# Kernel tuning notes

Measured on AMD Instinct MI355X. Metric: run time of the kernel, lower is better.

## Reference

```python
import jax, jax.numpy as jnp
import numpy as np

D_MODEL = 1024
EXPAND = 2
D_INNER = D_MODEL * EXPAND  # 2048
D_STATE = 16
D_CONV = 4
DT_RANK = max(16, D_MODEL // 16)  # 64
BATCH = 1
SEQ = 2048


def _hippo_eigvals(N):
    # HiPPO-LegS matrix: A[n,m] = -(2*max(n,m)+1)
    n = np.arange(N)
    A = -(2.0 * np.maximum(n[:, None], n[None, :]) + 1.0)
    w, _ = np.linalg.eigh(A)
    idx = np.argsort(np.abs(w))[::-1]
    return w[idx]


def setup_inputs() -> dict:
    key = jax.random.key(0)
    ks = jax.random.split(key, 10)
    s = 0.02
    return {
        "x": jax.random.normal(ks[0], (BATCH, SEQ, D_MODEL), jnp.float32),
        "in_w": jax.random.normal(ks[1], (D_MODEL, D_INNER), jnp.float32) * s,
        "in_b": jnp.zeros((D_INNER,), jnp.float32),
        "conv_w": jax.random.normal(ks[2], (D_INNER, 1, D_CONV), jnp.float32) * s,
        "conv_b": jnp.zeros((D_INNER,), jnp.float32),
        "A_log": jnp.asarray(np.log(np.abs(_hippo_eigvals(D_STATE))), jnp.float32),
        "B_mat": jax.random.normal(ks[3], (D_STATE, D_INNER), jnp.float32) * s,
        "C_mat": jax.random.normal(ks[4], (D_STATE, D_INNER), jnp.float32) * s,
        "D_vec": jnp.ones((D_INNER,), jnp.float32),
        "gate_w": jax.random.normal(ks[5], (D_MODEL, D_INNER), jnp.float32) * s,
        "gate_b": jnp.zeros((D_INNER,), jnp.float32),
        "dt1_w": jax.random.normal(ks[6], (D_INNER, DT_RANK), jnp.float32) * s,
        "dt1_b": jnp.zeros((DT_RANK,), jnp.float32),
        "dt2_w": jax.random.normal(ks[7], (DT_RANK, D_INNER), jnp.float32) * s,
        "dt2_b": jnp.full((D_INNER,), -4.0, jnp.float32),  # softplus -> small dt
        "out_w": jax.random.normal(ks[8], (D_INNER, D_MODEL), jnp.float32) * s,
        "out_b": jnp.zeros((D_MODEL,), jnp.float32),
    }


def reference(x, in_w, in_b, conv_w, conv_b, A_log, B_mat, C_mat, D_vec,
              gate_w, gate_b, dt1_w, dt1_b, dt2_w, dt2_b, out_w, out_b):
    B, L, _ = x.shape
    u = x @ in_w + in_b  # (B, L, D_INNER)
    # causal depthwise conv1d: left-pad d_conv-1 (torch pads both sides then trims to L)
    uc = jax.lax.conv_general_dilated(
        u.transpose(0, 2, 1), conv_w, (1,), [(D_CONV - 1, 0)],
        dimension_numbers=("NCH", "OIH", "NCH"),
        feature_group_count=D_INNER) + conv_b[None, :, None]
    u = jax.nn.silu(uc.transpose(0, 2, 1))  # (B, L, D_INNER)
    # input-dependent time step via low-rank dt projection
    delta = jax.nn.softplus((u @ dt1_w + dt1_b) @ dt2_w + dt2_b)  # (B, L, D_INNER)
    # ZOH discretization of diagonal A (matches discretize_zoh diagonal branch)
    A = -jnp.exp(A_log)  # (N,)
    dA = delta[..., None] * A  # (B, L, D, N)
    A_bar = jnp.exp(dA)
    safe_A = jnp.where(jnp.abs(A) < 1e-6, 1.0, A)
    expansion = jnp.where(jnp.abs(A) < 1e-6,
                          delta[..., None] * (1.0 + 0.5 * dA),
                          (A_bar - 1.0) / safe_A)  # (B, L, D, N)
    Bu = expansion * B_mat.T[None, None, :, :] * u[..., None]  # (B, L, D, N)
    # sequential state recurrence h[k] = A_bar[k] * h[k-1] + B_bar[k] * u[k]
    def step(h, ab_bu):
        ab, bu = ab_bu
        h = ab * h + bu
        return h, h
    h0 = jnp.zeros((B, D_INNER, D_STATE), x.dtype)
    _, hs = jax.lax.scan(step, h0, (A_bar.transpose(1, 0, 2, 3), Bu.transpose(1, 0, 2, 3)))
    hs = hs.transpose(1, 0, 2, 3)  # (B, L, D, N)
    y = jnp.einsum("bldn,nd->bld", hs, C_mat) + D_vec * u
    y = y * jax.nn.silu(x @ gate_w + gate_b)
    return y @ out_w + out_b
```

## Files before the change

kernel.cpp:

```cpp
#include <hip/hip_runtime.h>

#define L_SEQ 2048
#define DM    1024
#define DI    2048
#define NS    16
#define DTR   64
#define CH    128
#define CL    16
#define KZ_DT 16
#define KZ_OUT 4

typedef short bf16x8_t __attribute__((ext_vector_type(8)));
typedef float f32x4    __attribute__((ext_vector_type(4)));

__device__ __forceinline__ unsigned short f2bf(float f) {
    union { float f; unsigned int u; } v; v.f = f;
    unsigned int u = v.u;
    unsigned int r = (u + 0x7FFFu + ((u >> 16) & 1u)) >> 16;
    return (unsigned short)r;
}

__global__ void cast_bf16_kernel(const float* __restrict__ in,
                                 unsigned short* __restrict__ out, int n) {
    int i = (blockIdx.x * blockDim.x + threadIdx.x) * 4;
    if (i + 3 < n) {
        float4 v = *(const float4*)&in[i];
        ushort4 o;
        o.x = f2bf(v.x); o.y = f2bf(v.y); o.z = f2bf(v.z); o.w = f2bf(v.w);
        *(ushort4*)&out[i] = o;
    }
}

__global__ void tcast_kernel(const float* __restrict__ in,
                             unsigned short* __restrict__ out, int K, int N) {
    __shared__ float tile[32][33];
    int tx = threadIdx.x & 31, ty = threadIdx.x >> 5;
    int n0 = blockIdx.x * 32, k0 = blockIdx.y * 32;
    #pragma unroll
    for (int i = ty; i < 32; i += 8) {
        int k = k0 + i, n = n0 + tx;
        tile[i][tx] = (k < K && n < N) ? in[(size_t)k * N + n] : 0.f;
    }
    __syncthreads();
    #pragma unroll
    for (int i = ty; i < 32; i += 8) {
        int n = n0 + i, k = k0 + tx;
        if (n < N && k < K) out[(size_t)n * K + k] = f2bf(tile[tx][i]);
    }
}

__global__ __launch_bounds__(256, 2)
void gemm_bf16(const unsigned short* __restrict__ A,
               const unsigned short* __restrict__ Bt,
               float* __restrict__ C,
               const float* __restrict__ bias0, const float* __restrict__ bias1,
               int bsplit, int M, int Ntot, int K, int kchunk) {
    __shared__ short As[128][40];
    __shared__ short Bs[128][40];
    const int tid  = threadIdx.x;
    const int bm   = blockIdx.y * 128, bn = blockIdx.x * 128;
    const int lane = tid & 63, wave = tid >> 6;
    const int wm   = (wave >> 1) * 64, wn = (wave & 1) * 64;
    const int quad = lane >> 4, r16 = lane & 15;

    f32x4 acc[4][4];
    #pragma unroll
    for (int i = 0; i < 4; i++)
        #pragma unroll
        for (int j = 0; j < 4; j++)
            #pragma unroll
            for (int r = 0; r < 4; r++) acc[i][j][r] = 0.f;

    const int lrow = tid >> 2;
    const int lcol = (tid & 3) * 8;
    const short* agp = (const short*)A + (size_t)(bm + lrow) * K + lcol;
    const short* bgp = (const short*)Bt + (size_t)(bn + lrow) * K + lcol;
    const size_t rstep = (size_t)64 * K;

    const int kbase  = blockIdx.z * kchunk;
    const int kiters = kchunk / 32;

    int kcur = kbase;
    bf16x8_t na0 = *(const bf16x8_t*)(agp + kcur);
    bf16x8_t na1 = *(const bf16x8_t*)(agp + rstep + kcur);
    bf16x8_t nb0 = *(const bf16x8_t*)(bgp + kcur);
    bf16x8_t nb1 = *(const bf16x8_t*)(bgp + rstep + kcur);

    for (int it = 0; it < kiters; ++it) {
        *(bf16x8_t*)&As[lrow][lcol]      = na0;
        *(bf16x8_t*)&As[lrow + 64][lcol] = na1;
        *(bf16x8_t*)&Bs[lrow][lcol]      = nb0;
        *(bf16x8_t*)&Bs[lrow + 64][lcol] = nb1;
        __syncthreads();

        int kn = (it + 1 < kiters) ? kcur + 32 : kbase;
        kcur = kn;
        na0 = *(const bf16x8_t*)(agp + kn);
        na1 = *(const bf16x8_t*)(agp + rstep + kn);
        nb0 = *(const bf16x8_t*)(bgp + kn);
        nb1 = *(const bf16x8_t*)(bgp + rstep + kn);

        bf16x8_t af[4], bfr[4];
        #pragma unroll
        for (int i = 0; i < 4; i++)
            af[i] = *(const bf16x8_t*)&As[wm + i * 16 + r16][quad * 8];
        #pragma unroll
        for (int j = 0; j < 4; j++)
            bfr[j] = *(const bf16x8_t*)&Bs[wn + j * 16 + r16][quad * 8];
        #pragma unroll
        for (int i = 0; i < 4; i++)
            #pragma unroll
            for (int j = 0; j < 4; j++)
                acc[i][j] = __builtin_amdgcn_mfma_f32_16x16x32_bf16(
                    af[i], bfr[j], acc[i][j], 0, 0, 0);
        __syncthreads();
    }

    const bool partial = (gridDim.z > 1);
    float* Cw = C + (size_t)blockIdx.z * M * Ntot;
    #pragma unroll
    for (int i = 0; i < 4; i++)
        #pragma unroll
        for (int j = 0; j < 4; j++) {
            int col = bn + wn + j * 16 + r16;
            if (col < Ntot) {
                float bv = 0.f;
                if (!partial && bias0)
                    bv = (col < bsplit) ? bias0[col] : bias1[col - bsplit];
                #pragma unroll
                for (int r = 0; r < 4; r++) {
                    int row = bm + wm + i * 16 + quad * 4 + r;
                    Cw[(size_t)row * Ntot + col] = acc[i][j][r] + bv;
                }
            }
        }
}

__global__ void reduce_out_kernel(const float* __restrict__ part,
                                  const float* __restrict__ bias,
                                  float* __restrict__ out) {
    int i = (blockIdx.x * 256 + threadIdx.x) * 4;
    int col = i & (DM - 1);
    float4 s = *(const float4*)&part[i];
    #pragma unroll
    for (int z = 1; z < KZ_OUT; z++) {
        float4 p = *(const float4*)&part[(size_t)z * L_SEQ * DM + i];
        s.x += p.x; s.y += p.y; s.z += p.z; s.w += p.w;
    }
    float4 b = *(const float4*)&bias[col];
    s.x += b.x; s.y += b.y; s.z += b.z; s.w += b.w;
    *(float4*)&out[i] = s;
}

__global__ void conv_silu_kernel(const float* __restrict__ u0,
                                 const float* __restrict__ cw,
                                 const float* __restrict__ cb,
                                 float* __restrict__ uf,
                                 unsigned short* __restrict__ ub) {
    int d  = blockIdx.x * 256 + threadIdx.x;
    int l0 = blockIdx.y * 8;
    float4 w = *(const float4*)&cw[d * 4];
    float bias = cb[d];
    float x0 = 0.f, x1 = 0.f, x2 = 0.f;
    if (l0 >= 3) {
        x0 = u0[(size_t)(l0 - 3) * (2 * DI) + d];
        x1 = u0[(size_t)(l0 - 2) * (2 * DI) + d];
        x2 = u0[(size_t)(l0 - 1) * (2 * DI) + d];
    }
    #pragma unroll
    for (int t = 0; t < 8; t++) {
        float x3 = u0[(size_t)(l0 + t) * (2 * DI) + d];
        float s = bias + x0 * w.x + x1 * w.y + x2 * w.z + x3 * w.w;
        float sig = 1.f / (1.f + __expf(-s));
        float v = s * sig;
        uf[(size_t)(l0 + t) * DI + d] = v;
        ub[(size_t)(l0 + t) * DI + d] = f2bf(v);
        x0 = x1; x1 = x2; x2 = x3;
    }
}

__global__ void delta_kernel(const float* __restrict__ dtl_part,
                             const float* __restrict__ dt1b,
                             const float* __restrict__ dt2w,
                             const float* __restrict__ dt2b,
                             float* __restrict__ delta) {
    __shared__ float dl_s[8][64];
    int tid = threadIdx.x;
    int n   = blockIdx.x * 256 + tid;
    int m0  = blockIdx.y * 8;
    for (int idx = tid; idx < 512; idx += 256) {
        int r = idx >> 6, k = idx & 63;
        float s = dt1b[k];
        #pragma unroll
        for (int z = 0; z < KZ_DT; z++)
            s += dtl_part[((size_t)z * L_SEQ + m0 + r) * DTR + k];
        dl_s[r][k] = s;
    }
    __syncthreads();
    float acc[8] = {0, 0, 0, 0, 0, 0, 0, 0};
    for (int k = 0; k < 64; k++) {
        float w = dt2w[(size_t)k * DI + n];
        #pragma unroll
        for (int r = 0; r < 8; r++) acc[r] = fmaf(dl_s[r][k], w, acc[r]);
    }
    float b = dt2b[n];
    #pragma unroll
    for (int r = 0; r < 8; r++) {
        float v = acc[r] + b;
        float sp = (v > 15.f) ? v : log1pf(__expf(v));
        delta[(size_t)(m0 + r) * DI + n] = sp;
    }
}

__global__ __launch_bounds__(64)
void scan1_kernel(const float* __restrict__ delta,
                  const float* __restrict__ uf,
                  const float* __restrict__ A_log,
                  const float* __restrict__ Bm,
                  float* __restrict__ Aprod,
                  float* __restrict__ hend) {
    const int d = blockIdx.x * 64 + threadIdx.x;
    const int c = blockIdx.y;
    const int l0 = c * CL;
    float a[NS], iA[NS], Bn[NS];
    #pragma unroll
    for (int n = 0; n < NS; n++) {
        float av = -__expf(A_log[n]);
        a[n]  = av;
        iA[n] = (fabsf(av) < 1e-6f) ? 0.f : 1.f / av;
        Bn[n] = Bm[(size_t)n * DI + d];
    }
    float h[NS], P[NS];
    #pragma unroll
    for (int n = 0; n < NS; n++) { h[n] = 0.f; P[n] = 1.f; }

    float dl = delta[(size_t)l0 * DI + d];
    float ul = uf[(size_t)l0 * DI + d];
    #pragma unroll
    for (int t = 0; t < CL; t++) {
        float dln = 0.f, uln = 0.f;
        if (t + 1 < CL) {
            dln = delta[(size_t)(l0 + t + 1) * DI + d];
            uln = uf[(size_t)(l0 + t + 1) * DI + d];
        }
        #pragma unroll
        for (int n = 0; n < NS; n++) {
            float dA = dl * a[n];
            float ab = __expf(dA);
            float ex = (fabsf(a[n]) < 1e-6f) ? dl * fmaf(0.5f, dA, 1.f)
                                             : (ab - 1.f) * iA[n];
            float bu = ex * Bn[n] * ul;
            h[n] = fmaf(ab, h[n], bu);
            P[n] *= ab;
        }
        dl = dln; ul = uln;
    }
    size_t base = ((size_t)c * DI + d) * NS;
    #pragma unroll
    for (int q = 0; q < 4; q++) {
        *(float4*)&Aprod[base + q * 4] = make_float4(P[q*4], P[q*4+1], P[q*4+2], P[q*4+3]);
        *(float4*)&hend[base + q * 4]  = make_float4(h[q*4], h[q*4+1], h[q*4+2], h[q*4+3]);
    }
}

__global__ __launch_bounds__(64)
void combine_kernel(const float* __restrict__ Aprod,
                    const float* __restrict__ hend,
                    float* __restrict__ carry) {
    int t = blockIdx.x * 64 + threadIdx.x;
    float h = 0.f;
    for (int c = 0; c < CH; c++) {
        size_t idx = (size_t)c * (DI * NS) + t;
        carry[idx] = h;
        h = fmaf(Aprod[idx], h, hend[idx]);
    }
}

__global__ __launch_bounds__(64)
void scan2_kernel(const float* __restrict__ delta,
                  const float* __restrict__ uf,
                  const float* __restrict__ ug,
                  const float* __restrict__ A_log,
                  const float* __restrict__ Bm,
                  const float* __restrict__ Cm,
                  const float* __restrict__ Dv,
                  const float* __restrict__ carry,
                  unsigned short* __restrict__ yb) {
    const int d = blockIdx.x * 64 + threadIdx.x;
    const int c = blockIdx.y;
    const int l0 = c * CL;
    float a[NS], iA[NS], Bn[NS], Cn[NS], h[NS];
    #pragma unroll
    for (int n = 0; n < NS; n++) {
        float av = -__expf(A_log[n]);
        a[n]  = av;
        iA[n] = (fabsf(av) < 1e-6f) ? 0.f : 1.f / av;
        Bn[n] = Bm[(size_t)n * DI + d];
        Cn[n] = Cm[(size_t)n * DI + d];
    }
    float Dd = Dv[d];
    size_t cbase = ((size_t)c * DI + d) * NS;
    #pragma unroll
    for (int q = 0; q < 4; q++) {
        float4 cv = *(const float4*)&carry[cbase + q * 4];
        h[q*4] = cv.x; h[q*4+1] = cv.y; h[q*4+2] = cv.z; h[q*4+3] = cv.w;
    }

    float dl = delta[(size_t)l0 * DI + d];
    float ul = uf[(size_t)l0 * DI + d];
    float zr = ug[(size_t)l0 * (2 * DI) + DI + d];
    #pragma unroll
    for (int t = 0; t < CL; t++) {
        float dln = 0.f, uln = 0.f, zrn = 0.f;
        if (t + 1 < CL) {
            dln = delta[(size_t)(l0 + t + 1) * DI + d];
            uln = uf[(size_t)(l0 + t + 1) * DI + d];
            zrn = ug[(size_t)(l0 + t + 1) * (2 * DI) + DI + d];
        }
        float y = 0.f;
        #pragma unroll
        for (int n = 0; n < NS; n++) {
            float dA = dl * a[n];
            float ab = __expf(dA);
            float ex = (fabsf(a[n]) < 1e-6f) ? dl * fmaf(0.5f, dA, 1.f)
                                             : (ab - 1.f) * iA[n];
            float bu = ex * Bn[n] * ul;
            h[n] = fmaf(ab, h[n], bu);
            y = fmaf(h[n], Cn[n], y);
        }
        float ytot = fmaf(Dd, ul, y);
        float g = zr / (1.f + __expf(-zr));
        yb[(size_t)(l0 + t) * DI + d] = f2bf(ytot * g);
        dl = dln; ul = uln; zr = zrn;
    }
}

extern "C" void kernel_launch(void* const* d_in, const int* in_sizes, int n_in,
                              void* d_out, int out_size, void* d_ws, size_t ws_size,
                              hipStream_t stream) {
    const float* x      = (const float*)d_in[0];
    const float* in_w   = (const float*)d_in[1];
    const float* in_b   = (const float*)d_in[2];
    const float* conv_w = (const float*)d_in[3];
    const float* conv_b = (const float*)d_in[4];
    const float* A_log  = (const float*)d_in[5];
    const float* B_mat  = (const float*)d_in[6];
    const float* C_mat  = (const float*)d_in[7];
    const float* D_vec  = (const float*)d_in[8];
    const float* gate_w = (const float*)d_in[9];
    const float* gate_b = (const float*)d_in[10];
    const float* dt1_w  = (const float*)d_in[11];
    const float* dt1_b  = (const float*)d_in[12];
    const float* dt2_w  = (const float*)d_in[13];
    const float* dt2_b  = (const float*)d_in[14];
    const float* out_w  = (const float*)d_in[15];
    const float* out_b  = (const float*)d_in[16];

    char* ws = (char*)d_ws;
    size_t off = 0;
    auto alloc = [&](size_t bytes) {
        void* p = ws + off;
        off += (bytes + 255) & ~(size_t)255;
        return p;
    };

    unsigned short* xb     = (unsigned short*)alloc((size_t)L_SEQ * DM * 2);
    unsigned short* wtig   = (unsigned short*)alloc((size_t)2 * DI * DM * 2);
    unsigned short* out_wt = (unsigned short*)alloc((size_t)DM * DI * 2);
    unsigned short* dt1_wt = (unsigned short*)alloc((size_t)128 * DI * 2);
    float* ug      = (float*)alloc((size_t)L_SEQ * 2 * DI * 4);
    unsigned short* u_bf16 = (unsigned short*)alloc((size_t)L_SEQ * DI * 2);
    float* u_f32   = (float*)alloc((size_t)L_SEQ * DI * 4);
    float* dtl_p   = (float*)alloc((size_t)KZ_DT * L_SEQ * DTR * 4);
    float* delta   = (float*)alloc((size_t)L_SEQ * DI * 4);
    float* Aprod   = (float*)alloc((size_t)CH * DI * NS * 4);
    float* hend    = (float*)alloc((size_t)CH * DI * NS * 4);
    float* carry   = (float*)alloc((size_t)CH * DI * NS * 4);
    unsigned short* y_bf16  = (unsigned short*)dtl_p;
    float* out_part         = ug;
    (void)ws_size; (void)in_sizes; (void)n_in; (void)out_size;

    dim3 b256(256);

    cast_bf16_kernel<<<dim3((L_SEQ * DM) / 1024), b256, 0, stream>>>(x, xb, L_SEQ * DM);
    tcast_kernel<<<dim3(DI / 32, DM / 32), b256, 0, stream>>>(in_w, wtig, DM, DI);
    tcast_kernel<<<dim3(DI / 32, DM / 32), b256, 0, stream>>>(gate_w, wtig + (size_t)DI * DM, DM, DI);
    tcast_kernel<<<dim3(DM / 32, DI / 32), b256, 0, stream>>>(out_w, out_wt, DI, DM);
    tcast_kernel<<<dim3(DTR / 32, DI / 32), b256, 0, stream>>>(dt1_w, dt1_wt, DI, DTR);

    gemm_bf16<<<dim3(2 * DI / 128, L_SEQ / 128, 1), b256, 0, stream>>>(
        xb, wtig, ug, in_b, gate_b, DI, L_SEQ, 2 * DI, DM, DM);

    conv_silu_kernel<<<dim3(DI / 256, L_SEQ / 8), b256, 0, stream>>>(ug, conv_w, conv_b, u_f32, u_bf16);

    gemm_bf16<<<dim3(1, L_SEQ / 128, KZ_DT), b256, 0, stream>>>(
        u_bf16, dt1_wt, dtl_p, nullptr, nullptr, 0, L_SEQ, DTR, DI, DI / KZ_DT);

    delta_kernel<<<dim3(DI / 256, L_SEQ / 8), b256, 0, stream>>>(dtl_p, dt1_b, dt2_w, dt2_b, delta);

    scan1_kernel<<<dim3(DI / 64, CH), dim3(64), 0, stream>>>(delta, u_f32, A_log, B_mat, Aprod, hend);
    combine_kernel<<<dim3((DI * NS) / 64), dim3(64), 0, stream>>>(Aprod, hend, carry);
    scan2_kernel<<<dim3(DI / 64, CH), dim3(64), 0, stream>>>(delta, u_f32, ug, A_log, B_mat, C_mat,
                                                             D_vec, carry, y_bf16);

    gemm_bf16<<<dim3(DM / 128, L_SEQ / 128, KZ_OUT), b256, 0, stream>>>(
        y_bf16, out_wt, out_part, nullptr, nullptr, 0, L_SEQ, DM, DI, DI / KZ_OUT);
    reduce_out_kernel<<<dim3((L_SEQ * DM) / 1024), b256, 0, stream>>>(out_part, out_b, (float*)d_out);
}
```

Measured before the change: 290.1 us.

## Batch scan input loads, transpose chunk-state layout, widen scan blocks

Both scan kernels now load all 16 timesteps of delta, u and gate into registers before the recurrence, replacing the one-step-ahead prefetch. This is meant to expose more memory-level parallelism and hide load latency. The per-chunk state buffers (Aprod, hend, carry) change from [chunk][d][n] to [chunk][n][d], so stores and loads across threads are contiguous in d; the elementwise combine kernel works with either layout. Scan blocks also grow from 64 to 256 threads, and the extra preloaded registers may reduce occupancy.

```diff
diff --git a/kernel.cpp b/kernel.cpp
--- a/kernel.cpp
+++ b/kernel.cpp
@@ -212,16 +212,24 @@
     }
 }
 
-__global__ __launch_bounds__(64)
+__global__ __launch_bounds__(256)
 void scan1_kernel(const float* __restrict__ delta,
                   const float* __restrict__ uf,
                   const float* __restrict__ A_log,
                   const float* __restrict__ Bm,
                   float* __restrict__ Aprod,
                   float* __restrict__ hend) {
-    const int d = blockIdx.x * 64 + threadIdx.x;
+    const int d = blockIdx.x * 256 + threadIdx.x;
     const int c = blockIdx.y;
     const int l0 = c * CL;
+
+    float dl[CL], ul[CL];
+    #pragma unroll
+    for (int t = 0; t < CL; t++) {
+        dl[t] = delta[(size_t)(l0 + t) * DI + d];
+        ul[t] = uf[(size_t)(l0 + t) * DI + d];
+    }
+
     float a[NS], iA[NS], Bn[NS];
     #pragma unroll
     for (int n = 0; n < NS; n++) {
@@ -234,32 +242,24 @@
     #pragma unroll
     for (int n = 0; n < NS; n++) { h[n] = 0.f; P[n] = 1.f; }
 
-    float dl = delta[(size_t)l0 * DI + d];
-    float ul = uf[(size_t)l0 * DI + d];
     #pragma unroll
     for (int t = 0; t < CL; t++) {
-        float dln = 0.f, uln = 0.f;
-        if (t + 1 < CL) {
-            dln = delta[(size_t)(l0 + t + 1) * DI + d];
-            uln = uf[(size_t)(l0 + t + 1) * DI + d];
-        }
         #pragma unroll
         for (int n = 0; n < NS; n++) {
-            float dA = dl * a[n];
+            float dA = dl[t] * a[n];
             float ab = __expf(dA);
-            float ex = (fabsf(a[n]) < 1e-6f) ? dl * fmaf(0.5f, dA, 1.f)
+            float ex = (fabsf(a[n]) < 1e-6f) ? dl[t] * fmaf(0.5f, dA, 1.f)
                                              : (ab - 1.f) * iA[n];
-            float bu = ex * Bn[n] * ul;
+            float bu = ex * Bn[n] * ul[t];
             h[n] = fmaf(ab, h[n], bu);
             P[n] *= ab;
         }
-        dl = dln; ul = uln;
-    }
-    size_t base = ((size_t)c * DI + d) * NS;
-    #pragma unroll
-    for (int q = 0; q < 4; q++) {
-        *(float4*)&Aprod[base + q * 4] = make_float4(P[q*4], P[q*4+1], P[q*4+2], P[q*4+3]);
-        *(float4*)&hend[base + q * 4]  = make_float4(h[q*4], h[q*4+1], h[q*4+2], h[q*4+3]);
+    }
+    #pragma unroll
+    for (int n = 0; n < NS; n++) {
+        size_t idx = ((size_t)c * NS + n) * DI + d;
+        Aprod[idx] = P[n];
+        hend[idx]  = h[n];
     }
 }
 
@@ -276,7 +276,7 @@
     }
 }
 
-__global__ __launch_bounds__(64)
+__global__ __launch_bounds__(256)
 void scan2_kernel(const float* __restrict__ delta,
                   const float* __restrict__ uf,
                   const float* __restrict__ ug,
@@ -286,9 +286,18 @@
                   const float* __restrict__ Dv,
                   const float* __restrict__ carry,
                   unsigned short* __restrict__ yb) {
-    const int d = blockIdx.x * 64 + threadIdx.x;
+    const int d = blockIdx.x * 256 + threadIdx.x;
     const int c = blockIdx.y;
     const int l0 = c * CL;
+
+    float dl[CL], ul[CL], zr[CL];
+    #pragma unroll
+    for (int t = 0; t < CL; t++) {
+        dl[t] = delta[(size_t)(l0 + t) * DI + d];
+        ul[t] = uf[(size_t)(l0 + t) * DI + d];
+        zr[t] = ug[(size_t)(l0 + t) * (2 * DI) + DI + d];
+    }
+
     float a[NS], iA[NS], Bn[NS], Cn[NS], h[NS];
     #pragma unroll
     for (int n = 0; n < NS; n++) {
@@ -297,41 +306,26 @@
         iA[n] = (fabsf(av) < 1e-6f) ? 0.f : 1.f / av;
         Bn[n] = Bm[(size_t)n * DI + d];
         Cn[n] = Cm[(size_t)n * DI + d];
+        h[n]  = carry[((size_t)c * NS + n) * DI + d];
     }
     float Dd = Dv[d];
-    size_t cbase = ((size_t)c * DI + d) * NS;
-    #pragma unroll
-    for (int q = 0; q < 4; q++) {
-        float4 cv = *(const float4*)&carry[cbase + q * 4];
-        h[q*4] = cv.x; h[q*4+1] = cv.y; h[q*4+2] = cv.z; h[q*4+3] = cv.w;
-    }
-
-    float dl = delta[(size_t)l0 * DI + d];
-    float ul = uf[(size_t)l0 * DI + d];
-    float zr = ug[(size_t)l0 * (2 * DI) + DI + d];
+
     #pragma unroll
     for (int t = 0; t < CL; t++) {
-        float dln = 0.f, uln = 0.f, zrn = 0.f;
-        if (t + 1 < CL) {
-            dln = delta[(size_t)(l0 + t + 1) * DI + d];
-            uln = uf[(size_t)(l0 + t + 1) * DI + d];
-            zrn = ug[(size_t)(l0 + t + 1) * (2 * DI) + DI + d];
-        }
         float y = 0.f;
         #pragma unroll
         for (int n = 0; n < NS; n++) {
-            float dA = dl * a[n];
+            float dA = dl[t] * a[n];
             float ab = __expf(dA);
-            float ex = (fabsf(a[n]) < 1e-6f) ? dl * fmaf(0.5f, dA, 1.f)
+            float ex = (fabsf(a[n]) < 1e-6f) ? dl[t] * fmaf(0.5f, dA, 1.f)
                                              : (ab - 1.f) * iA[n];
-            float bu = ex * Bn[n] * ul;
+            float bu = ex * Bn[n] * ul[t];
             h[n] = fmaf(ab, h[n], bu);
             y = fmaf(h[n], Cn[n], y);
         }
-        float ytot = fmaf(Dd, ul, y);
-        float g = zr / (1.f + __expf(-zr));
+        float ytot = fmaf(Dd, ul[t], y);
+        float g = zr[t] / (1.f + __expf(-zr[t]));
         yb[(size_t)(l0 + t) * DI + d] = f2bf(ytot * g);
-        dl = dln; ul = uln; zr = zrn;
     }
 }
 
@@ -398,10 +392,10 @@
 
     delta_kernel<<<dim3(DI / 256, L_SEQ / 8), b256, 0, stream>>>(dtl_p, dt1_b, dt2_w, dt2_b, delta);
 
-    scan1_kernel<<<dim3(DI / 64, CH), dim3(64), 0, stream>>>(delta, u_f32, A_log, B_mat, Aprod, hend);
+    scan1_kernel<<<dim3(DI / 256, CH), b256, 0, stream>>>(delta, u_f32, A_log, B_mat, Aprod, hend);
     combine_kernel<<<dim3((DI * NS) / 64), dim3(64), 0, stream>>>(Aprod, hend, carry);
-    scan2_kernel<<<dim3(DI / 64, CH), dim3(64), 0, stream>>>(delta, u_f32, ug, A_log, B_mat, C_mat,
-                                                             D_vec, carry, y_bf16);
+    scan2_kernel<<<dim3(DI / 256, CH), b256, 0, stream>>>(delta, u_f32, ug, A_log, B_mat, C_mat,
+                                                          D_vec, carry, y_bf16);
 
     gemm_bf16<<<dim3(DM / 128, L_SEQ / 128, KZ_OUT), b256, 0, stream>>>(
         y_bf16, out_wt, out_part, nullptr, nullptr, 0, L_SEQ, DM, DI, DI / KZ_OUT);
```

Result: slower. 322.0 us (+11.0%).
